# Performance work log

Measured on AMD Instinct MI355X. Metric: run time of the kernel, lower is better.

The kernel has to match this reference:

```python
import jax, jax.numpy as jnp
import numpy as np

# dims: B batch, T obs_length, NOV num_ov, N nodes, F feature size, NF node feat, EF edge feat
B, T, NOV, N, F, NF, EF = 32, 10, 3, 128, 16, 5, 2
C = NOV + 1      # c_size channels in GCN
SL = 2           # stack_length of gcn_module1 (repo default assumption)
HID = N * F      # critic/actor hidden


def setup_inputs() -> dict:
    key = jax.random.key(0)
    ks = jax.random.split(key, 20)
    s = 0.05
    return {
        "inputs": jax.random.uniform(ks[0], (B, T * NOV, N, 3 * N + NF), dtype=jnp.float32),
        "We": jax.random.normal(ks[1], (EF, F), dtype=jnp.float32) * s,
        "be": jax.random.normal(ks[2], (F,), dtype=jnp.float32) * s,
        "Wn": jax.random.normal(ks[3], (NF, F), dtype=jnp.float32) * s,
        "bn": jax.random.normal(ks[4], (F,), dtype=jnp.float32) * s,
        "Wg": jax.random.normal(ks[5], (SL, C, F, F), dtype=jnp.float32) * s,   # per-layer per-channel linear weights
        "bgl": jax.random.normal(ks[6], (SL, C, F), dtype=jnp.float32) * s,     # per-layer per-channel linear biases
        "gbias": jax.random.normal(ks[7], (C, 1, F), dtype=jnp.float32) * s,    # GNN_module.bias
        "Wc1": jax.random.normal(ks[8], (C * N * F, HID), dtype=jnp.float32) * s,
        "bc1": jax.random.normal(ks[9], (HID,), dtype=jnp.float32) * s,
        "Wc2": jax.random.normal(ks[10], (HID, F), dtype=jnp.float32) * s,
        "bc2": jax.random.normal(ks[11], (F,), dtype=jnp.float32) * s,
        "Wc3": jax.random.normal(ks[12], (F, 1), dtype=jnp.float32) * s,
        "bc3": jax.random.normal(ks[13], (1,), dtype=jnp.float32) * s,
        "Wa1": jax.random.normal(ks[14], (C * N * F, HID), dtype=jnp.float32) * s,
        "ba1": jax.random.normal(ks[15], (HID,), dtype=jnp.float32) * s,
        "Wa2": jax.random.normal(ks[16], (HID, F), dtype=jnp.float32) * s,
        "ba2": jax.random.normal(ks[17], (F,), dtype=jnp.float32) * s,
    }


def _gcn(adj, x, Wg, bgl, gbias):
    # adj: [M,N,N]; x: [M,C,N,F_in]. Faithful to GNN_module.forward with add_loop=True.
    n = adj.shape[1]
    i = jnp.arange(n)
    a = adj.at[:, i, i].set(1.0)  # self loops
    for l in range(Wg.shape[0]):
        c_in = x.shape[1]
        # lin_i(x).sum(dim=1) for each output channel i; bias summed over c_in channels
        y = jnp.einsum('bcnf,ifo->bino', x, Wg[l]) + c_in * bgl[l][None, :, None, :]
        # degree re-normalization each stack layer (as in original)
        deg = jnp.clip(a.sum(-1), 1.0) ** -0.5
        a = deg[:, :, None] * a * deg[:, None, :]
        x = jax.nn.leaky_relu(jnp.einsum('bnm,bcmo->bcno', a, y) + gbias)
    return x


def reference(inputs, We, be, Wn, bn, Wg, bgl, gbias,
              Wc1, bc1, Wc2, bc2, Wc3, bc3, Wa1, ba1, Wa2, ba2):
    b = inputs.shape[0]
    adj = inputs[:, 0, :, :N]                                   # [b,N,N]
    edge = inputs[:, 0, :, N:3 * N].reshape(b, N, N, EF)        # [b,N,N,2]
    node = inputs[:, :, :, 3 * N:].reshape(b, T, NOV, N, NF)    # [b,T,NOV,N,5]

    edge_enc = (jax.nn.leaky_relu(edge @ We + be) * adj[..., None]).sum(axis=1)  # [b,N,F]
    node_enc = jax.nn.leaky_relu(node @ Wn + bn)                                 # [b,T,NOV,N,F]

    # encode loop over t vectorized by folding t into batch
    feats = jnp.concatenate(
        [jnp.broadcast_to(edge_enc[:, None, None], (b, T, 1, N, F)), node_enc], axis=2
    )                                                            # [b,T,C,N,F]
    adj_rep = jnp.broadcast_to(adj[:, None], (b, T, N, N)).reshape(b * T, N, N)
    g = _gcn(adj_rep, feats.reshape(b * T, C, N, F), Wg, bgl, gbias)
    graph = g.reshape(b, T, C, N, F).sum(axis=1)                 # out accumulated over obs_length

    flat = graph.reshape(b, -1)                                  # [b, C*N*F]
    h = jax.nn.leaky_relu(flat @ Wc1 + bc1)
    h = jax.nn.leaky_relu(h @ Wc2 + bc2)
    critic = h @ Wc3 + bc3                                       # [b,1]
    ha = jax.nn.leaky_relu(flat @ Wa1 + ba1)
    actor = jax.nn.leaky_relu(ha @ Wa2 + ba2)                    # [b,F]
    return (critic, actor)
```

## Files before the change

### kernel.cpp

```cpp
#include <hip/hip_runtime.h>
#include <stdint.h>

#define LEAKY(x) ((x) > 0.f ? (x) : 0.01f*(x))

typedef __attribute__((ext_vector_type(8))) short bf16x8;
typedef __attribute__((ext_vector_type(4))) float f32x4;

__device__ __forceinline__ unsigned short f2bf(float x){
  unsigned u = __float_as_uint(x);
  u += 0x7FFFu + ((u >> 16) & 1u);
  return (unsigned short)(u >> 16);
}
__device__ __forceinline__ void fma4(float4& a, float s, const float4& w){
  a.x = fmaf(s, w.x, a.x); a.y = fmaf(s, w.y, a.y);
  a.z = fmaf(s, w.z, a.z); a.w = fmaf(s, w.w, a.w);
}
__device__ __forceinline__ float dot16(const float* __restrict__ xn, const float* wg, float a){
  float4 x0 = *(const float4*)(xn);
  float4 x1 = *(const float4*)(xn+4);
  float4 x2 = *(const float4*)(xn+8);
  float4 x3 = *(const float4*)(xn+12);
  a = fmaf(x0.x, wg[0], a);  a = fmaf(x0.y, wg[1], a);  a = fmaf(x0.z, wg[2], a);  a = fmaf(x0.w, wg[3], a);
  a = fmaf(x1.x, wg[4], a);  a = fmaf(x1.y, wg[5], a);  a = fmaf(x1.z, wg[6], a);  a = fmaf(x1.w, wg[7], a);
  a = fmaf(x2.x, wg[8], a);  a = fmaf(x2.y, wg[9], a);  a = fmaf(x2.z, wg[10], a); a = fmaf(x2.w, wg[11], a);
  a = fmaf(x3.x, wg[12], a); a = fmaf(x3.y, wg[13], a); a = fmaf(x3.z, wg[14], a); a = fmaf(x3.w, wg[15], a);
  return a;
}

__global__ __launch_bounds__(256) void k_edge(const float* __restrict__ inp,
                                              const float* __restrict__ We,
                                              const float* __restrict__ be,
                                              float* __restrict__ edge_enc){
  int b = blockIdx.x >> 3, jg = blockIdx.x & 7;
  int t = threadIdx.x;
  int j = jg*16 + (t >> 4), f = t & 15;
  const float* base = inp + (size_t)b*30*128*389;
  float w0 = We[f], w1 = We[16+f], bf = be[f];
  float acc = 0.f;
  for (int i = 0; i < 128; ++i){
    const float* row = base + i*389;
    float adjv = row[j];
    float2 e = *(const float2*)(row + 128 + 2*j);
    float v = fmaf(e.x, w0, fmaf(e.y, w1, bf));
    v = LEAKY(v);
    acc = fmaf(v, adjv, acc);
  }
  edge_enc[b*2048 + j*16 + f] = acc;
}

__global__ __launch_bounds__(256) void k_prep(const float* __restrict__ inp,
                                              unsigned short* __restrict__ A1b,
                                              unsigned short* __restrict__ A2b){
  __shared__ float As[128*129];
  __shared__ float ps[256];
  __shared__ float dg[128];
  int b = blockIdx.x, t = threadIdx.x;
  const float* base = inp + (size_t)b*30*128*389;
  for (int idx = t; idx < 16384; idx += 256){
    int n = idx >> 7, m = idx & 127;
    As[n*129 + m] = base[n*389 + m];
  }
  __syncthreads();
  if (t < 128) As[t*129 + t] = 1.0f;
  __syncthreads();
  for (int pass = 0; pass < 2; ++pass){
    int n = t >> 1, h = t & 1;
    float s = 0.f;
    for (int m = h*64; m < h*64 + 64; ++m) s += As[n*129 + m];
    ps[t] = s;
    __syncthreads();
    if (t < 128) dg[t] = rsqrtf(fmaxf(ps[2*t] + ps[2*t+1], 1.0f));
    __syncthreads();
    unsigned short* dst = pass ? A2b : A1b;
    for (int idx = t; idx < 16384; idx += 256){
      int nn = idx >> 7, m = idx & 127;
      float v = dg[nn] * As[nn*129 + m] * dg[m];
      if (!pass) As[nn*129 + m] = v;
      dst[b*16384 + idx] = f2bf(v);
    }
    __syncthreads();
  }
}

__global__ __launch_bounds__(256) void k_nodeS(const float* __restrict__ inp,
                                               const float* __restrict__ Wn,
                                               const float* __restrict__ bn,
                                               float* __restrict__ S){
  __shared__ float WnL[80];
  __shared__ float bnL[16];
  int t = threadIdx.x;
  if (t < 80) WnL[t] = Wn[t];
  if (t < 16) bnL[t] = bn[t];
  __syncthreads();
  int id = blockIdx.x*256 + t;
  int b = id / 1280, rem = id % 1280;
  int tt = rem >> 7, n = rem & 127;
  float outv[16];
  #pragma unroll
  for (int f = 0; f < 16; ++f) outv[f] = 0.f;
  for (int v = 0; v < 3; ++v){
    const float* row = inp + (size_t)((b*30 + tt*3 + v)*128 + n)*389 + 384;
    float x0 = row[0], x1 = row[1], x2 = row[2], x3 = row[3], x4 = row[4];
    #pragma unroll
    for (int f = 0; f < 16; ++f){
      float a = bnL[f];
      a = fmaf(x0, WnL[f], a);
      a = fmaf(x1, WnL[16+f], a);
      a = fmaf(x2, WnL[32+f], a);
      a = fmaf(x3, WnL[48+f], a);
      a = fmaf(x4, WnL[64+f], a);
      outv[f] += LEAKY(a);
    }
  }
  float* dst = S + (size_t)((b*10 + tt)*128 + n)*16;
  #pragma unroll
  for (int q = 0; q < 4; ++q)
    *(float4*)(dst + q*4) = make_float4(outv[q*4], outv[q*4+1], outv[q*4+2], outv[q*4+3]);
}

__global__ __launch_bounds__(256) void k_gcn(const float* __restrict__ edge_enc,
                                             const float* __restrict__ S,
                                             const unsigned short* __restrict__ A1b,
                                             const unsigned short* __restrict__ A2b,
                                             const float* __restrict__ Wg,
                                             const float* __restrict__ bgl,
                                             const float* __restrict__ gbias,
                                             float* __restrict__ graph){
  __shared__ __align__(16) unsigned short Af[128*136];
  __shared__ __align__(16) unsigned short YT[64*136];
  __shared__ __align__(16) float xsb[128*16];
  int blk = blockIdx.x;
  int b = blk/10, tt = blk%10;
  int t = threadIdx.x, lane = t & 63, wave = t >> 6;
  int io = lane, ic = io >> 4, o = io & 15;
  int lo = lane & 15, qd = lane >> 4;

  float wg0[16], wg1[16];
  #pragma unroll
  for (int f = 0; f < 16; ++f){
    wg0[f] = Wg[(ic*16 + f)*16 + o];
    wg1[f] = Wg[((4 + ic)*16 + f)*16 + o];
  }
  float bg0 = 4.f * bgl[ic*16 + o];
  float bg1 = 4.f * bgl[64 + ic*16 + o];
  float gb[4];
  #pragma unroll
  for (int q = 0; q < 4; ++q) gb[q] = gbias[q*16 + lo];

  uint4 areg[8];
  {
    const uint4* gA = (const uint4*)(A1b + b*16384);
    #pragma unroll
    for (int q = 0; q < 8; ++q) areg[q] = gA[q*256 + t];
  }
  {
    const float4* ge = (const float4*)(edge_enc + b*2048);
    const float4* gs = (const float4*)(S + (size_t)(b*10 + tt)*2048);
    float4* xf = (float4*)xsb;
    float4 a0 = ge[2*t], s0 = gs[2*t];
    float4 a1 = ge[2*t+1], s1 = gs[2*t+1];
    xf[2*t]   = make_float4(a0.x+s0.x, a0.y+s0.y, a0.z+s0.z, a0.w+s0.w);
    xf[2*t+1] = make_float4(a1.x+s1.x, a1.y+s1.y, a1.z+s1.z, a1.w+s1.w);
  }
  __syncthreads();

  #pragma unroll
  for (int nb = 0; nb < 32; nb += 8){
    unsigned pk[4];
    #pragma unroll
    for (int u = 0; u < 8; ++u){
      int n = wave*32 + nb + u;
      float a = dot16(&xsb[n*16], wg0, bg0);
      unsigned short hb = f2bf(a);
      if (u & 1) pk[u>>1] |= ((unsigned)hb) << 16; else pk[u>>1] = (unsigned)hb;
    }
    *(uint4*)&YT[io*136 + wave*32 + nb] = make_uint4(pk[0], pk[1], pk[2], pk[3]);
  }
  #pragma unroll
  for (int q = 0; q < 8; ++q){
    int c = q*256 + t;
    *(uint4*)&Af[(c >> 4)*136 + (c & 15)*8] = areg[q];
  }
  __syncthreads();

  f32x4 acc0[2][4];
  #pragma unroll
  for (int mi = 0; mi < 2; ++mi)
    #pragma unroll
    for (int nt = 0; nt < 4; ++nt) acc0[mi][nt] = (f32x4){0.f,0.f,0.f,0.f};
  #pragma unroll
  for (int kt = 0; kt < 4; ++kt){
    bf16x8 av[2], bv[4];
    #pragma unroll
    for (int mi = 0; mi < 2; ++mi)
      av[mi] = *(const bf16x8*)&Af[(wave*32 + mi*16 + lo)*136 + kt*32 + qd*8];
    #pragma unroll
    for (int nt = 0; nt < 4; ++nt)
      bv[nt] = *(const bf16x8*)&YT[(nt*16 + lo)*136 + kt*32 + qd*8];
    #pragma unroll
    for (int mi = 0; mi < 2; ++mi)
      #pragma unroll
      for (int nt = 0; nt < 4; ++nt)
        acc0[mi][nt] = __builtin_amdgcn_mfma_f32_16x16x32_bf16(av[mi], bv[nt], acc0[mi][nt], 0, 0, 0);
  }
  {
    const uint4* gA = (const uint4*)(A2b + b*16384);
    #pragma unroll
    for (int q = 0; q < 8; ++q) areg[q] = gA[q*256 + t];
  }
  #pragma unroll
  for (int mi = 0; mi < 2; ++mi)
    #pragma unroll
    for (int r = 0; r < 4; ++r){
      float s = 0.f;
      #pragma unroll
      for (int nt = 0; nt < 4; ++nt){
        float v = acc0[mi][nt][r] + gb[nt];
        s += LEAKY(v);
      }
      int n = wave*32 + mi*16 + qd*4 + r;
      xsb[n*16 + lo] = s;
    }
  __syncthreads();

  #pragma unroll
  for (int nb = 0; nb < 32; nb += 8){
    unsigned pk[4];
    #pragma unroll
    for (int u = 0; u < 8; ++u){
      int n = wave*32 + nb + u;
      float a = dot16(&xsb[n*16], wg1, bg1);
      unsigned short hb = f2bf(a);
      if (u & 1) pk[u>>1] |= ((unsigned)hb) << 16; else pk[u>>1] = (unsigned)hb;
    }
    *(uint4*)&YT[io*136 + wave*32 + nb] = make_uint4(pk[0], pk[1], pk[2], pk[3]);
  }
  #pragma unroll
  for (int q = 0; q < 8; ++q){
    int c = q*256 + t;
    *(uint4*)&Af[(c >> 4)*136 + (c & 15)*8] = areg[q];
  }
  __syncthreads();

  f32x4 acc1[2][4];
  #pragma unroll
  for (int mi = 0; mi < 2; ++mi)
    #pragma unroll
    for (int nt = 0; nt < 4; ++nt) acc1[mi][nt] = (f32x4){0.f,0.f,0.f,0.f};
  #pragma unroll
  for (int kt = 0; kt < 4; ++kt){
    bf16x8 av[2], bv[4];
    #pragma unroll
    for (int mi = 0; mi < 2; ++mi)
      av[mi] = *(const bf16x8*)&Af[(wave*32 + mi*16 + lo)*136 + kt*32 + qd*8];
    #pragma unroll
    for (int nt = 0; nt < 4; ++nt)
      bv[nt] = *(const bf16x8*)&YT[(nt*16 + lo)*136 + kt*32 + qd*8];
    #pragma unroll
    for (int mi = 0; mi < 2; ++mi)
      #pragma unroll
      for (int nt = 0; nt < 4; ++nt)
        acc1[mi][nt] = __builtin_amdgcn_mfma_f32_16x16x32_bf16(av[mi], bv[nt], acc1[mi][nt], 0, 0, 0);
  }
  float* gout = graph + (size_t)b*8192;
  #pragma unroll
  for (int mi = 0; mi < 2; ++mi)
    #pragma unroll
    for (int nt = 0; nt < 4; ++nt)
      #pragma unroll
      for (int r = 0; r < 4; ++r){
        float v = acc1[mi][nt][r] + gb[nt];
        v = LEAKY(v);
        int n = wave*32 + mi*16 + qd*4 + r;
        atomicAdd(&gout[nt*2048 + n*16 + lo], v);
      }
}

__global__ __launch_bounds__(256) void k_gemm(const float* __restrict__ graph,
                                              const float* __restrict__ Wc1,
                                              const float* __restrict__ Wa1,
                                              float* __restrict__ part){
  __shared__ __align__(16) float flatc[32*256];
  __shared__ __align__(16) float Wt[16*256];
  int bx = blockIdx.x;
  int ks = bx >> 4, cb = bx & 15;
  const float* W = (cb < 8) ? Wc1 : Wa1;
  int cw0 = (cb & 7) * 256;
  int k0 = ks * 256;
  int t = threadIdx.x, lane = t & 63, wave = t >> 6;
  #pragma unroll
  for (int q = 0; q < 8; ++q){
    int idx4 = t + 256*q; int r = idx4 >> 6, c4 = idx4 & 63;
    *(float4*)&flatc[r*256 + c4*4] = *(const float4*)(graph + (size_t)r*8192 + k0 + c4*4);
  }
  float4 acc4[8];
  #pragma unroll
  for (int i = 0; i < 8; ++i) acc4[i] = make_float4(0.f,0.f,0.f,0.f);
  float4 stg[4];
  #pragma unroll
  for (int q = 0; q < 4; ++q){
    int idx4 = t + 256*q; int s = idx4 >> 6, c4 = idx4 & 63;
    stg[q] = *(const float4*)(W + (size_t)(k0 + s)*2048 + cw0 + c4*4);
  }
  int r0 = wave*8, c0l = lane*4;
  for (int j = 0; j < 16; ++j){
    asm volatile("s_waitcnt lgkmcnt(0)\ns_barrier" ::: "memory");
    #pragma unroll
    for (int q = 0; q < 4; ++q){
      int idx4 = t + 256*q; int s = idx4 >> 6, c4 = idx4 & 63;
      *(float4*)&Wt[s*256 + c4*4] = stg[q];
    }
    if (j < 15){
      #pragma unroll
      for (int q = 0; q < 4; ++q){
        int idx4 = t + 256*q; int s = idx4 >> 6, c4 = idx4 & 63;
        stg[q] = *(const float4*)(W + (size_t)(k0 + (j+1)*16 + s)*2048 + cw0 + c4*4);
      }
    }
    asm volatile("s_waitcnt lgkmcnt(0)\ns_barrier" ::: "memory");
    #pragma unroll
    for (int kk4 = 0; kk4 < 4; ++kk4){
      float4 wv0 = *(const float4*)&Wt[(kk4*4+0)*256 + c0l];
      float4 wv1 = *(const float4*)&Wt[(kk4*4+1)*256 + c0l];
      float4 wv2 = *(const float4*)&Wt[(kk4*4+2)*256 + c0l];
      float4 wv3 = *(const float4*)&Wt[(kk4*4+3)*256 + c0l];
      #pragma unroll
      for (int ii = 0; ii < 8; ++ii){
        float4 fvv = *(const float4*)&flatc[(r0+ii)*256 + j*16 + kk4*4];
        fma4(acc4[ii], fvv.x, wv0);
        fma4(acc4[ii], fvv.y, wv1);
        fma4(acc4[ii], fvv.z, wv2);
        fma4(acc4[ii], fvv.w, wv3);
      }
    }
  }
  float* dst = part + (size_t)ks*131072 + cb*256 + c0l;
  #pragma unroll
  for (int ii = 0; ii < 8; ++ii)
    *(float4*)(dst + (size_t)(r0+ii)*4096) = acc4[ii];
}

__global__ __launch_bounds__(256) void k_reduce(const float* __restrict__ part,
                                                const float* __restrict__ bc1,
                                                const float* __restrict__ ba1,
                                                float* __restrict__ hcomb){
  int id = blockIdx.x*256 + threadIdx.x;
  float s = 0.f;
  #pragma unroll 8
  for (int p = 0; p < 32; ++p) s += part[(size_t)p*131072 + id];
  int c = id & 4095;
  s += (c < 2048) ? bc1[c] : ba1[c - 2048];
  hcomb[id] = LEAKY(s);
}

__global__ __launch_bounds__(256) void k_heads(const float* __restrict__ hcomb,
                                               const float* __restrict__ Wc2,
                                               const float* __restrict__ bc2,
                                               const float* __restrict__ Wc3,
                                               const float* __restrict__ bc3,
                                               const float* __restrict__ Wa2,
                                               const float* __restrict__ ba2,
                                               float* __restrict__ out){
  __shared__ float red[256*17];
  int r = blockIdx.x >> 1, which = blockIdx.x & 1;
  int t = threadIdx.x;
  const float* x = hcomb + r*4096 + which*2048;
  const float* W2 = which ? Wa2 : Wc2;
  float acc[16];
  #pragma unroll
  for (int f = 0; f < 16; ++f) acc[f] = 0.f;
  for (int k = t; k < 2048; k += 256){
    float xv = x[k];
    const float4* wr = (const float4*)(W2 + k*16);
    float4 w0 = wr[0], w1 = wr[1], w2 = wr[2], w3 = wr[3];
    acc[0]  = fmaf(xv, w0.x, acc[0]);  acc[1]  = fmaf(xv, w0.y, acc[1]);
    acc[2]  = fmaf(xv, w0.z, acc[2]);  acc[3]  = fmaf(xv, w0.w, acc[3]);
    acc[4]  = fmaf(xv, w1.x, acc[4]);  acc[5]  = fmaf(xv, w1.y, acc[5]);
    acc[6]  = fmaf(xv, w1.z, acc[6]);  acc[7]  = fmaf(xv, w1.w, acc[7]);
    acc[8]  = fmaf(xv, w2.x, acc[8]);  acc[9]  = fmaf(xv, w2.y, acc[9]);
    acc[10] = fmaf(xv, w2.z, acc[10]); acc[11] = fmaf(xv, w2.w, acc[11]);
    acc[12] = fmaf(xv, w3.x, acc[12]); acc[13] = fmaf(xv, w3.y, acc[13]);
    acc[14] = fmaf(xv, w3.z, acc[14]); acc[15] = fmaf(xv, w3.w, acc[15]);
  }
  #pragma unroll
  for (int f = 0; f < 16; ++f) red[t*17 + f] = acc[f];
  __syncthreads();
  for (int off = 128; off >= 1; off >>= 1){
    if (t < off){
      #pragma unroll
      for (int f = 0; f < 16; ++f) red[t*17 + f] += red[(t+off)*17 + f];
    }
    __syncthreads();
  }
  if (which == 0){
    if (t == 0){
      float c = bc3[0];
      #pragma unroll
      for (int f = 0; f < 16; ++f){
        float v = red[f] + bc2[f];
        v = LEAKY(v);
        c = fmaf(v, Wc3[f], c);
      }
      out[r] = c;
    }
  } else {
    if (t < 16){
      float v = red[t] + ba2[t];
      out[32 + r*16 + t] = LEAKY(v);
    }
  }
}

static const size_t O_EDGE  = 0;
static const size_t O_S     = 262144;
static const size_t O_A1    = 2883584;
static const size_t O_A2    = 3932160;
static const size_t O_GRAPH = 4980736;
static const size_t O_PART  = 6029312;
static const size_t O_HC    = 22806528;

extern "C" void kernel_launch(void* const* d_in, const int* in_sizes, int n_in,
                              void* d_out, int out_size, void* d_ws, size_t ws_size,
                              hipStream_t stream){
  const float* inp  = (const float*)d_in[0];
  const float* We   = (const float*)d_in[1];
  const float* be   = (const float*)d_in[2];
  const float* Wn   = (const float*)d_in[3];
  const float* bn   = (const float*)d_in[4];
  const float* Wg   = (const float*)d_in[5];
  const float* bgl  = (const float*)d_in[6];
  const float* gbias= (const float*)d_in[7];
  const float* Wc1  = (const float*)d_in[8];
  const float* bc1  = (const float*)d_in[9];
  const float* Wc2  = (const float*)d_in[10];
  const float* bc2  = (const float*)d_in[11];
  const float* Wc3  = (const float*)d_in[12];
  const float* bc3  = (const float*)d_in[13];
  const float* Wa1  = (const float*)d_in[14];
  const float* ba1  = (const float*)d_in[15];
  const float* Wa2  = (const float*)d_in[16];
  const float* ba2  = (const float*)d_in[17];

  char* ws = (char*)d_ws;
  float* edge_enc      = (float*)(ws + O_EDGE);
  float* S             = (float*)(ws + O_S);
  unsigned short* A1b  = (unsigned short*)(ws + O_A1);
  unsigned short* A2b  = (unsigned short*)(ws + O_A2);
  float* graph         = (float*)(ws + O_GRAPH);
  float* part          = (float*)(ws + O_PART);
  float* hcomb         = (float*)(ws + O_HC);

  hipMemsetAsync(graph, 0, 262144*sizeof(float), stream);
  hipLaunchKernelGGL(k_edge,   dim3(256), dim3(256), 0, stream, inp, We, be, edge_enc);
  hipLaunchKernelGGL(k_prep,   dim3(32),  dim3(256), 0, stream, inp, A1b, A2b);
  hipLaunchKernelGGL(k_nodeS,  dim3(160), dim3(256), 0, stream, inp, Wn, bn, S);
  hipLaunchKernelGGL(k_gcn,    dim3(320), dim3(256), 0, stream, edge_enc, S, A1b, A2b, Wg, bgl, gbias, graph);
  hipLaunchKernelGGL(k_gemm,   dim3(512), dim3(256), 0, stream, graph, Wc1, Wa1, part);
  hipLaunchKernelGGL(k_reduce, dim3(512), dim3(256), 0, stream, part, bc1, ba1, hcomb);
  hipLaunchKernelGGL(k_heads,  dim3(64),  dim3(256), 0, stream, hcomb, Wc2, bc2, Wc3, bc3, Wa2, ba2, (float*)d_out);
}
```

Measured before the change: 409.3 us.

## Merge prep kernels, replace atomics with per-timestep buffer and sum, fold reduce into heads

Merges the edge-encoding, adjacency normalization and node-encoding kernels into one launch that splits work by block index. The GCN kernel now writes per-timestep outputs instead of doing atomicAdd into a zeroed buffer, and a new k_sum kernel adds the ten timesteps, which removes the memset and the atomic contention. The split-K reduce of the first dense layer is moved into the heads kernel, dropping one launch and the hcomb round trip. In exchange it adds a 10 MB intermediate write and read, and the reduction in heads runs on only 64 blocks, which may be less parallel than the old 512-block reduce.

```diff
diff --git a/kernel.cpp b/kernel.cpp
--- a/kernel.cpp
+++ b/kernel.cpp
@@ -27,95 +27,92 @@
   return a;
 }
 
-__global__ __launch_bounds__(256) void k_edge(const float* __restrict__ inp,
-                                              const float* __restrict__ We,
-                                              const float* __restrict__ be,
-                                              float* __restrict__ edge_enc){
-  int b = blockIdx.x >> 3, jg = blockIdx.x & 7;
-  int t = threadIdx.x;
-  int j = jg*16 + (t >> 4), f = t & 15;
-  const float* base = inp + (size_t)b*30*128*389;
-  float w0 = We[f], w1 = We[16+f], bf = be[f];
-  float acc = 0.f;
-  for (int i = 0; i < 128; ++i){
-    const float* row = base + i*389;
-    float adjv = row[j];
-    float2 e = *(const float2*)(row + 128 + 2*j);
-    float v = fmaf(e.x, w0, fmaf(e.y, w1, bf));
-    v = LEAKY(v);
-    acc = fmaf(v, adjv, acc);
-  }
-  edge_enc[b*2048 + j*16 + f] = acc;
-}
-
-__global__ __launch_bounds__(256) void k_prep(const float* __restrict__ inp,
-                                              unsigned short* __restrict__ A1b,
-                                              unsigned short* __restrict__ A2b){
-  __shared__ float As[128*129];
-  __shared__ float ps[256];
-  __shared__ float dg[128];
-  int b = blockIdx.x, t = threadIdx.x;
-  const float* base = inp + (size_t)b*30*128*389;
-  for (int idx = t; idx < 16384; idx += 256){
-    int n = idx >> 7, m = idx & 127;
-    As[n*129 + m] = base[n*389 + m];
-  }
-  __syncthreads();
-  if (t < 128) As[t*129 + t] = 1.0f;
-  __syncthreads();
-  for (int pass = 0; pass < 2; ++pass){
-    int n = t >> 1, h = t & 1;
-    float s = 0.f;
-    for (int m = h*64; m < h*64 + 64; ++m) s += As[n*129 + m];
-    ps[t] = s;
+__global__ __launch_bounds__(256) void k_stage1(const float* __restrict__ inp,
+                                                const float* __restrict__ We,
+                                                const float* __restrict__ be,
+                                                const float* __restrict__ Wn,
+                                                const float* __restrict__ bn,
+                                                float* __restrict__ edge_enc,
+                                                unsigned short* __restrict__ A1b,
+                                                unsigned short* __restrict__ A2b,
+                                                float* __restrict__ S){
+  __shared__ float sm[16896];
+  int bx = blockIdx.x, t = threadIdx.x;
+
+  if (bx < 256){
+    int b = bx >> 3, jg = bx & 7;
+    int j = jg*16 + (t >> 4), f = t & 15;
+    const float* base = inp + (size_t)b*30*128*389;
+    float w0 = We[f], w1 = We[16+f], bf = be[f];
+    float acc = 0.f;
+    #pragma unroll 4
+    for (int i = 0; i < 128; ++i){
+      const float* row = base + i*389;
+      float adjv = row[j];
+      float2 e = *(const float2*)(row + 128 + 2*j);
+      float v = fmaf(e.x, w0, fmaf(e.y, w1, bf));
+      v = LEAKY(v);
+      acc = fmaf(v, adjv, acc);
+    }
+    edge_enc[b*2048 + j*16 + f] = acc;
+  } else if (bx < 288){
+    float* As = sm; float* ps = sm + 16512; float* dg = sm + 16768;
+    int b = bx - 256;
+    const float* base = inp + (size_t)b*30*128*389;
+    for (int idx = t; idx < 16384; idx += 256){
+      int n = idx >> 7, m = idx & 127;
+      As[n*129 + m] = base[n*389 + m];
+    }
     __syncthreads();
-    if (t < 128) dg[t] = rsqrtf(fmaxf(ps[2*t] + ps[2*t+1], 1.0f));
+    if (t < 128) As[t*129 + t] = 1.0f;
     __syncthreads();
-    unsigned short* dst = pass ? A2b : A1b;
-    for (int idx = t; idx < 16384; idx += 256){
-      int nn = idx >> 7, m = idx & 127;
-      float v = dg[nn] * As[nn*129 + m] * dg[m];
-      if (!pass) As[nn*129 + m] = v;
-      dst[b*16384 + idx] = f2bf(v);
-    }
+    for (int pass = 0; pass < 2; ++pass){
+      int n = t >> 1, h = t & 1;
+      float s = 0.f;
+      for (int m = h*64; m < h*64 + 64; ++m) s += As[n*129 + m];
+      ps[t] = s;
+      __syncthreads();
+      if (t < 128) dg[t] = rsqrtf(fmaxf(ps[2*t] + ps[2*t+1], 1.0f));
+      __syncthreads();
+      unsigned short* dst = pass ? A2b : A1b;
+      for (int idx = t; idx < 16384; idx += 256){
+        int nn = idx >> 7, m = idx & 127;
+        float v = dg[nn] * As[nn*129 + m] * dg[m];
+        if (!pass) As[nn*129 + m] = v;
+        dst[b*16384 + idx] = f2bf(v);
+      }
+      __syncthreads();
+    }
+  } else {
+    float* WnL = sm; float* bnL = sm + 80;
+    if (t < 80) WnL[t] = Wn[t];
+    if (t < 16) bnL[t] = bn[t];
     __syncthreads();
-  }
-}
-
-__global__ __launch_bounds__(256) void k_nodeS(const float* __restrict__ inp,
-                                               const float* __restrict__ Wn,
-                                               const float* __restrict__ bn,
-                                               float* __restrict__ S){
-  __shared__ float WnL[80];
-  __shared__ float bnL[16];
-  int t = threadIdx.x;
-  if (t < 80) WnL[t] = Wn[t];
-  if (t < 16) bnL[t] = bn[t];
-  __syncthreads();
-  int id = blockIdx.x*256 + t;
-  int b = id / 1280, rem = id % 1280;
-  int tt = rem >> 7, n = rem & 127;
-  float outv[16];
-  #pragma unroll
-  for (int f = 0; f < 16; ++f) outv[f] = 0.f;
-  for (int v = 0; v < 3; ++v){
-    const float* row = inp + (size_t)((b*30 + tt*3 + v)*128 + n)*389 + 384;
-    float x0 = row[0], x1 = row[1], x2 = row[2], x3 = row[3], x4 = row[4];
-    #pragma unroll
-    for (int f = 0; f < 16; ++f){
-      float a = bnL[f];
-      a = fmaf(x0, WnL[f], a);
-      a = fmaf(x1, WnL[16+f], a);
-      a = fmaf(x2, WnL[32+f], a);
-      a = fmaf(x3, WnL[48+f], a);
-      a = fmaf(x4, WnL[64+f], a);
-      outv[f] += LEAKY(a);
-    }
-  }
-  float* dst = S + (size_t)((b*10 + tt)*128 + n)*16;
-  #pragma unroll
-  for (int q = 0; q < 4; ++q)
-    *(float4*)(dst + q*4) = make_float4(outv[q*4], outv[q*4+1], outv[q*4+2], outv[q*4+3]);
+    int id = (bx - 288)*256 + t;
+    int b = id / 1280, rem = id % 1280;
+    int tt = rem >> 7, n = rem & 127;
+    float outv[16];
+    #pragma unroll
+    for (int f = 0; f < 16; ++f) outv[f] = 0.f;
+    for (int v = 0; v < 3; ++v){
+      const float* row = inp + (size_t)((b*30 + tt*3 + v)*128 + n)*389 + 384;
+      float x0 = row[0], x1 = row[1], x2 = row[2], x3 = row[3], x4 = row[4];
+      #pragma unroll
+      for (int f = 0; f < 16; ++f){
+        float a = bnL[f];
+        a = fmaf(x0, WnL[f], a);
+        a = fmaf(x1, WnL[16+f], a);
+        a = fmaf(x2, WnL[32+f], a);
+        a = fmaf(x3, WnL[48+f], a);
+        a = fmaf(x4, WnL[64+f], a);
+        outv[f] += LEAKY(a);
+      }
+    }
+    float* dst = S + (size_t)((b*10 + tt)*128 + n)*16;
+    #pragma unroll
+    for (int q = 0; q < 4; ++q)
+      *(float4*)(dst + q*4) = make_float4(outv[q*4], outv[q*4+1], outv[q*4+2], outv[q*4+3]);
+  }
 }
 
 __global__ __launch_bounds__(256) void k_gcn(const float* __restrict__ edge_enc,
@@ -125,7 +122,7 @@
                                              const float* __restrict__ Wg,
                                              const float* __restrict__ bgl,
                                              const float* __restrict__ gbias,
-                                             float* __restrict__ graph){
+                                             float* __restrict__ g10){
   __shared__ __align__(16) unsigned short Af[128*136];
   __shared__ __align__(16) unsigned short YT[64*136];
   __shared__ __align__(16) float xsb[128*16];
@@ -262,7 +259,7 @@
       for (int nt = 0; nt < 4; ++nt)
         acc1[mi][nt] = __builtin_amdgcn_mfma_f32_16x16x32_bf16(av[mi], bv[nt], acc1[mi][nt], 0, 0, 0);
   }
-  float* gout = graph + (size_t)b*8192;
+  float* gout = g10 + (size_t)(b*10 + tt)*8192;
   #pragma unroll
   for (int mi = 0; mi < 2; ++mi)
     #pragma unroll
@@ -272,8 +269,23 @@
         float v = acc1[mi][nt][r] + gb[nt];
         v = LEAKY(v);
         int n = wave*32 + mi*16 + qd*4 + r;
-        atomicAdd(&gout[nt*2048 + n*16 + lo], v);
-      }
+        gout[nt*2048 + n*16 + lo] = v;
+      }
+}
+
+__global__ __launch_bounds__(256) void k_sum(const float* __restrict__ g10,
+                                             float* __restrict__ graph){
+  int blk = blockIdx.x;
+  int b = blk >> 3, seg = blk & 7;
+  int t = threadIdx.x;
+  size_t off = (size_t)seg*1024 + t*4;
+  float4 a = make_float4(0.f,0.f,0.f,0.f);
+  #pragma unroll
+  for (int tt = 0; tt < 10; ++tt){
+    float4 v = *(const float4*)(g10 + (size_t)(b*10 + tt)*8192 + off);
+    a.x += v.x; a.y += v.y; a.z += v.z; a.w += v.w;
+  }
+  *(float4*)(graph + (size_t)b*8192 + off) = a;
 }
 
 __global__ __launch_bounds__(256) void k_gemm(const float* __restrict__ graph,
@@ -340,20 +352,9 @@
     *(float4*)(dst + (size_t)(r0+ii)*4096) = acc4[ii];
 }
 
-__global__ __launch_bounds__(256) void k_reduce(const float* __restrict__ part,
-                                                const float* __restrict__ bc1,
-                                                const float* __restrict__ ba1,
-                                                float* __restrict__ hcomb){
-  int id = blockIdx.x*256 + threadIdx.x;
-  float s = 0.f;
-  #pragma unroll 8
-  for (int p = 0; p < 32; ++p) s += part[(size_t)p*131072 + id];
-  int c = id & 4095;
-  s += (c < 2048) ? bc1[c] : ba1[c - 2048];
-  hcomb[id] = LEAKY(s);
-}
-
-__global__ __launch_bounds__(256) void k_heads(const float* __restrict__ hcomb,
+__global__ __launch_bounds__(256) void k_heads(const float* __restrict__ part,
+                                               const float* __restrict__ bc1,
+                                               const float* __restrict__ ba1,
                                                const float* __restrict__ Wc2,
                                                const float* __restrict__ bc2,
                                                const float* __restrict__ Wc3,
@@ -364,13 +365,18 @@
   __shared__ float red[256*17];
   int r = blockIdx.x >> 1, which = blockIdx.x & 1;
   int t = threadIdx.x;
-  const float* x = hcomb + r*4096 + which*2048;
   const float* W2 = which ? Wa2 : Wc2;
+  const float* b1 = which ? ba1 : bc1;
+  const float* pbase = part + (size_t)r*4096 + which*2048;
   float acc[16];
   #pragma unroll
   for (int f = 0; f < 16; ++f) acc[f] = 0.f;
   for (int k = t; k < 2048; k += 256){
-    float xv = x[k];
+    float s = 0.f;
+    #pragma unroll 8
+    for (int p = 0; p < 32; ++p) s += pbase[(size_t)p*131072 + k];
+    s += b1[k];
+    float xv = LEAKY(s);
     const float4* wr = (const float4*)(W2 + k*16);
     float4 w0 = wr[0], w1 = wr[1], w2 = wr[2], w3 = wr[3];
     acc[0]  = fmaf(xv, w0.x, acc[0]);  acc[1]  = fmaf(xv, w0.y, acc[1]);
@@ -415,9 +421,9 @@
 static const size_t O_S     = 262144;
 static const size_t O_A1    = 2883584;
 static const size_t O_A2    = 3932160;
-static const size_t O_GRAPH = 4980736;
-static const size_t O_PART  = 6029312;
-static const size_t O_HC    = 22806528;
+static const size_t O_G10   = 4980736;
+static const size_t O_GRAPH = 15466496;
+static const size_t O_PART  = 16515072;
 
 extern "C" void kernel_launch(void* const* d_in, const int* in_sizes, int n_in,
                               void* d_out, int out_size, void* d_ws, size_t ws_size,
@@ -446,16 +452,13 @@
   float* S             = (float*)(ws + O_S);
   unsigned short* A1b  = (unsigned short*)(ws + O_A1);
   unsigned short* A2b  = (unsigned short*)(ws + O_A2);
+  float* g10           = (float*)(ws + O_G10);
   float* graph         = (float*)(ws + O_GRAPH);
   float* part          = (float*)(ws + O_PART);
-  float* hcomb         = (float*)(ws + O_HC);
-
-  hipMemsetAsync(graph, 0, 262144*sizeof(float), stream);
-  hipLaunchKernelGGL(k_edge,   dim3(256), dim3(256), 0, stream, inp, We, be, edge_enc);
-  hipLaunchKernelGGL(k_prep,   dim3(32),  dim3(256), 0, stream, inp, A1b, A2b);
-  hipLaunchKernelGGL(k_nodeS,  dim3(160), dim3(256), 0, stream, inp, Wn, bn, S);
-  hipLaunchKernelGGL(k_gcn,    dim3(320), dim3(256), 0, stream, edge_enc, S, A1b, A2b, Wg, bgl, gbias, graph);
+
+  hipLaunchKernelGGL(k_stage1, dim3(448), dim3(256), 0, stream, inp, We, be, Wn, bn, edge_enc, A1b, A2b, S);
+  hipLaunchKernelGGL(k_gcn,    dim3(320), dim3(256), 0, stream, edge_enc, S, A1b, A2b, Wg, bgl, gbias, g10);
+  hipLaunchKernelGGL(k_sum,    dim3(256), dim3(256), 0, stream, g10, graph);
   hipLaunchKernelGGL(k_gemm,   dim3(512), dim3(256), 0, stream, graph, Wc1, Wa1, part);
-  hipLaunchKernelGGL(k_reduce, dim3(512), dim3(256), 0, stream, part, bc1, ba1, hcomb);
-  hipLaunchKernelGGL(k_heads,  dim3(64),  dim3(256), 0, stream, hcomb, Wc2, bc2, Wc3, bc3, Wa2, ba2, (float*)d_out);
-}
+  hipLaunchKernelGGL(k_heads,  dim3(64),  dim3(256), 0, stream, part, bc1, ba1, Wc2, bc2, Wc3, bc3, Wa2, ba2, (float*)d_out);
+}
```

New measurement: 403.6 us. No clear change (-1.4%).
